# Kernel tuning notes

Hardware: AMD Instinct MI355X
Metric: run time of the kernel (lower is better)

## Reference

```python
import jax, jax.numpy as jnp
import numpy as np

N = 100000
E = 1600000
IN_CH = 64
HID = 32


def _gatv2(x, src, dst, wl, bl, wr, br, att, bias, heads, out_ch, concat):
    # GATv2Conv (PyG semantics, share_weights=False, negative_slope=0.2,
    # self-loops already appended to src/dst by caller).
    n = x.shape[0]
    xl = (x @ wl + bl).reshape(n, heads, out_ch)  # source transform
    xr = (x @ wr + br).reshape(n, heads, out_ch)  # target transform
    xj = xl[src]                                   # [E, H, C]
    xi = xr[dst]
    e = jax.nn.leaky_relu(xi + xj, negative_slope=0.2)
    alpha = jnp.einsum('ehc,hc->eh', e, att)       # [E, H]
    amax = jax.ops.segment_max(alpha, dst, num_segments=n)
    alpha = jnp.exp(alpha - amax[dst])
    denom = jax.ops.segment_sum(alpha, dst, num_segments=n)
    alpha = alpha / (denom[dst] + 1e-16)
    out = jax.ops.segment_sum(alpha[:, :, None] * xj, dst, num_segments=n)
    out = out.reshape(n, heads * out_ch) if concat else out.mean(axis=1)
    return out + bias


def setup_inputs() -> dict:
    key = jax.random.key(0)
    ks = jax.random.split(key, 20)
    s = 0.1
    d = {
        'x': jax.random.normal(ks[0], (N, IN_CH), jnp.float32),
        'edge_index': jax.random.randint(ks[1], (2, E), 0, N, jnp.int32),
        # conv1: in=64 -> heads=4, C=32, concat
        'w1l': s * jax.random.normal(ks[2], (IN_CH, 4 * HID), jnp.float32),
        'b1l': jnp.zeros((4 * HID,), jnp.float32),
        'w1r': s * jax.random.normal(ks[3], (IN_CH, 4 * HID), jnp.float32),
        'b1r': jnp.zeros((4 * HID,), jnp.float32),
        'a1': s * jax.random.normal(ks[4], (4, HID), jnp.float32),
        'c1': jnp.zeros((4 * HID,), jnp.float32),
        # conv2: in=128 -> heads=2, C=32, concat
        'w2l': s * jax.random.normal(ks[5], (4 * HID, 2 * HID), jnp.float32),
        'b2l': jnp.zeros((2 * HID,), jnp.float32),
        'w2r': s * jax.random.normal(ks[6], (4 * HID, 2 * HID), jnp.float32),
        'b2r': jnp.zeros((2 * HID,), jnp.float32),
        'a2': s * jax.random.normal(ks[7], (2, HID), jnp.float32),
        'c2': jnp.zeros((2 * HID,), jnp.float32),
        # conv3: in=64 -> heads=1, C=32, mean (concat=False)
        'w3l': s * jax.random.normal(ks[8], (2 * HID, HID), jnp.float32),
        'b3l': jnp.zeros((HID,), jnp.float32),
        'w3r': s * jax.random.normal(ks[9], (2 * HID, HID), jnp.float32),
        'b3r': jnp.zeros((HID,), jnp.float32),
        'a3': s * jax.random.normal(ks[10], (1, HID), jnp.float32),
        'c3': jnp.zeros((HID,), jnp.float32),
        # MLP head 32 -> 16 -> 2
        'wm1': s * jax.random.normal(ks[11], (HID, HID // 2), jnp.float32),
        'bm1': jnp.zeros((HID // 2,), jnp.float32),
        'wm2': s * jax.random.normal(ks[12], (HID // 2, 2), jnp.float32),
        'bm2': jnp.zeros((2,), jnp.float32),
    }
    return d


def reference(x, edge_index,
              w1l, b1l, w1r, b1r, a1, c1,
              w2l, b2l, w2r, b2r, a2, c2,
              w3l, b3l, w3r, b3r, a3, c3,
              wm1, bm1, wm2, bm2):
    n = x.shape[0]
    loop = jnp.arange(n, dtype=edge_index.dtype)
    src = jnp.concatenate([edge_index[0], loop])  # add_self_loops=True (PyG default)
    dst = jnp.concatenate([edge_index[1], loop])
    h = jax.nn.relu(_gatv2(x, src, dst, w1l, b1l, w1r, b1r, a1, c1, 4, HID, True))
    h = jax.nn.relu(_gatv2(h, src, dst, w2l, b2l, w2r, b2r, a2, c2, 2, HID, True))
    h = jax.nn.relu(_gatv2(h, src, dst, w3l, b3l, w3r, b3r, a3, c3, 1, HID, False))
    raw = jax.nn.relu(h @ wm1 + bm1) @ wm2 + bm2
    v_mag = jax.nn.sigmoid(raw[:, 0]) + 0.5
    v_angle = jnp.tanh(raw[:, 1]) * 180.0
    return jnp.stack([v_mag, v_angle], axis=1)
```

## Files before the change

### kernel.cpp

```cpp
#include <hip/hip_runtime.h>
#include <hip/hip_fp16.h>


constexpr int N = 100000;
constexpr int E = 1600000;
constexpr int S = 48;

constexpr int NBUK = (N + 127) >> 7;
constexpr int BCAP = 384;
constexpr int EPB = 8192;
constexpr int BIN_B = (E + EPB - 1) / EPB;
constexpr int XMM_B = (N + 127) / 128;

typedef _Float16 half8_t __attribute__((ext_vector_type(8)));
typedef _Float16 half4_t __attribute__((ext_vector_type(4)));
typedef _Float16 h2 __attribute__((ext_vector_type(2)));
typedef float f32x4 __attribute__((ext_vector_type(4)));


template <int NT>
__device__ __forceinline__ void bin_body(const int* __restrict__ ei,
                                         int* __restrict__ bcnt,
                                         unsigned* __restrict__ bbuf,
                                         int blk, int cls) {
  __shared__ int hist[NBUK];
  const int tid = threadIdx.x;
  const int e0 = blk * EPB;
  for (int i = tid; i < NBUK; i += NT) hist[i] = 0;
  __syncthreads();
  #pragma unroll 4
  for (int j = 0; j < EPB / NT; ++j) {
    const int e = e0 + j * NT + tid;
    if (e < E) atomicAdd(&hist[ei[E + e] >> 7], 1);
  }
  __syncthreads();
  for (int i = tid; i < NBUK; i += NT) {
    const int h = hist[i];
    hist[i] = h ? atomicAdd(&bcnt[i * 8 + cls], h) : 0;
  }
  __syncthreads();
  #pragma unroll 4
  for (int j = 0; j < EPB / NT; ++j) {
    const int e = e0 + j * NT + tid;
    if (e < E) {
      const int src = ei[e];
      const int dst = ei[E + e];
      const int b = dst >> 7;
      const int pos = atomicAdd(&hist[b], 1);
      if (pos < BCAP)
        bbuf[(size_t)(b * 8 + cls) * BCAP + pos] =
            ((unsigned)(dst & 127) << 17) | (unsigned)src;
    }
  }
}


__global__ __launch_bounds__(256) void k_insert(const int* __restrict__ bcnt,
                                                const unsigned* __restrict__ bbuf,
                                                int* __restrict__ deg,
                                                int* __restrict__ ebuf) {
  __shared__ int cnt[128];
  const int b = blockIdx.x;
  const int tid = threadIdx.x;
  const int node0 = b * 128 + tid;
  if (tid < 128) {
    cnt[tid] = 1;
    if (node0 < N) ebuf[node0 * S] = node0;
  }
  __syncthreads();
  #pragma unroll 1
  for (int c = 0; c < 8; ++c) {
    const int n = min(bcnt[b * 8 + c], BCAP);
    const unsigned* arr = bbuf + (size_t)(b * 8 + c) * BCAP;
    for (int i = tid; i < n; i += 256) {
      const unsigned ent = arr[i];
      const int dlo = (int)(ent >> 17);
      const int src = (int)(ent & 0x1FFFFu);
      const int pos = atomicAdd(&cnt[dlo], 1);
      if (pos < S) ebuf[(b * 128 + dlo) * S + pos] = src;
    }
  }
  __syncthreads();
  if (tid < 128 && node0 < N) deg[node0] = cnt[tid];
}


template <int K, int M>
__device__ __forceinline__ void wprep_body(const float* __restrict__ src,
                                           __half* __restrict__ dst, int blk) {
  const int idx = blk * 256 + threadIdx.x;
  const int k = idx / M;
  const int m = idx % M;
  ((_Float16*)dst)[m * K + (k ^ ((m & 7) << 3))] = (_Float16)src[idx];
}

__global__ __launch_bounds__(256) void k_wprep(
    const float* w1l, const float* w1r, const float* w2l, const float* w2r,
    const float* w3l, const float* w3r,
    __half* o1l, __half* o1r, __half* o2l, __half* o2r,
    __half* o3l, __half* o3r) {
  int b = blockIdx.x;
  if      (b < 32)  wprep_body<64, 128>(w1l, o1l, b);
  else if (b < 64)  wprep_body<64, 128>(w1r, o1r, b - 32);
  else if (b < 96)  wprep_body<128, 64>(w2l, o2l, b - 64);
  else if (b < 128) wprep_body<128, 64>(w2r, o2r, b - 96);
  else if (b < 136) wprep_body<64, 32>(w3l, o3l, b - 128);
  else              wprep_body<64, 32>(w3r, o3r, b - 136);
}


template <int K, int M, bool FP16IN>
__device__ __forceinline__ void xmm_body(const void* __restrict__ xin,
                                         const __half* __restrict__ wtl,
                                         const __half* __restrict__ wtr,
                                         const float* __restrict__ bl,
                                         const float* __restrict__ br,
                                         __half* __restrict__ Aout,
                                         __half* __restrict__ Bout, int blk) {
  constexpr int NPB = 128;
  constexpr int XSZ = NPB * K;
  constexpr int WSZ = M * K;
  constexpr int KS = K / 32;
  constexpr int CT = M / 16;
  constexpr int PSZ = (XSZ + 2 * WSZ) > (NPB * M) ? (XSZ + 2 * WSZ) : (NPB * M);
  __shared__ _Float16 pool[PSZ];

  const int tid = threadIdx.x;
  const int node0 = blk * NPB;

  if constexpr (!FP16IN) {
    const float* x = (const float*)xin;
    for (int i = tid; i < NPB * (K / 4); i += 512) {
      const int row = i / (K / 4);
      const int c4 = i % (K / 4);
      const int grow = min(node0 + row, N - 1);
      float4 v = reinterpret_cast<const float4*>(x)[(size_t)grow * (K / 4) + c4];
      const int k0 = c4 * 4;
      const int hidx = row * K + (k0 ^ ((row & 7) << 3));
      *reinterpret_cast<half4_t*>(&pool[hidx]) =
          (half4_t){(_Float16)v.x, (_Float16)v.y, (_Float16)v.z, (_Float16)v.w};
    }
  } else {
    const uint4* x = (const uint4*)xin;
    for (int i = tid; i < NPB * (K / 8); i += 512) {
      const int row = i / (K / 8);
      const int c8 = i % (K / 8);
      const int grow = min(node0 + row, N - 1);
      uint4 v = x[(size_t)grow * (K / 8) + c8];
      const int k0 = c8 * 8;
      *reinterpret_cast<uint4*>(&pool[row * K + (k0 ^ ((row & 7) << 3))]) = v;
    }
  }
  for (int i = tid; i < WSZ / 8; i += 512) {
    reinterpret_cast<uint4*>(&pool[XSZ])[i] =
        reinterpret_cast<const uint4*>(wtl)[i];
    reinterpret_cast<uint4*>(&pool[XSZ + WSZ])[i] =
        reinterpret_cast<const uint4*>(wtr)[i];
  }
  __syncthreads();

  const int lane = tid & 63;
  const int wid = tid >> 6;
  const int r0 = wid * 16;

  half8_t af[KS];
  #pragma unroll
  for (int ks = 0; ks < KS; ++ks) {
    const int row = r0 + (lane & 15);
    const int k0 = ks * 32 + (lane >> 4) * 8;
    af[ks] = *reinterpret_cast<const half8_t*>(
        &pool[row * K + (k0 ^ ((row & 7) << 3))]);
  }

  f32x4 accl[CT], accr[CT];
  #pragma unroll
  for (int ct = 0; ct < CT; ++ct) {
    accl[ct] = (f32x4){0.f, 0.f, 0.f, 0.f};
    accr[ct] = (f32x4){0.f, 0.f, 0.f, 0.f};
  }

  #pragma unroll
  for (int ct = 0; ct < CT; ++ct) {
    #pragma unroll
    for (int ks = 0; ks < KS; ++ks) {
      const int col = ct * 16 + (lane & 15);
      const int k0 = ks * 32 + (lane >> 4) * 8;
      const int hb = col * K + (k0 ^ ((col & 7) << 3));
      half8_t bfl = *reinterpret_cast<const half8_t*>(&pool[XSZ + hb]);
      accl[ct] = __builtin_amdgcn_mfma_f32_16x16x32_f16(af[ks], bfl, accl[ct], 0, 0, 0);
      half8_t bfr = *reinterpret_cast<const half8_t*>(&pool[XSZ + WSZ + hb]);
      accr[ct] = __builtin_amdgcn_mfma_f32_16x16x32_f16(af[ks], bfr, accr[ct], 0, 0, 0);
    }
  }

  __syncthreads();
  #pragma unroll
  for (int ct = 0; ct < CT; ++ct) {
    const int col = ct * 16 + (lane & 15);
    const float bb = bl[col];
    #pragma unroll
    for (int r = 0; r < 4; ++r) {
      const int row = r0 + (lane >> 4) * 4 + r;
      pool[row * M + col] = (_Float16)(accl[ct][r] + bb);
    }
  }
  __syncthreads();
  for (int i = tid; i < NPB * (M / 8); i += 512) {
    const int row = i / (M / 8);
    const int j = i % (M / 8);
    const int g = node0 + row;
    if (g < N)
      reinterpret_cast<uint4*>(Aout + (size_t)g * M)[j] =
          reinterpret_cast<uint4*>(&pool[row * M])[j];
  }
  __syncthreads();
  #pragma unroll
  for (int ct = 0; ct < CT; ++ct) {
    const int col = ct * 16 + (lane & 15);
    const float bb = br[col];
    #pragma unroll
    for (int r = 0; r < 4; ++r) {
      const int row = r0 + (lane >> 4) * 4 + r;
      pool[row * M + col] = (_Float16)(accr[ct][r] + bb);
    }
  }
  __syncthreads();
  for (int i = tid; i < NPB * (M / 8); i += 512) {
    const int row = i / (M / 8);
    const int j = i % (M / 8);
    const int g = node0 + row;
    if (g < N)
      reinterpret_cast<uint4*>(Bout + (size_t)g * M)[j] =
          reinterpret_cast<uint4*>(&pool[row * M])[j];
  }
}


__global__ __launch_bounds__(512) void k_front(const float* __restrict__ x,
                                               const __half* __restrict__ t1l,
                                               const __half* __restrict__ t1r,
                                               const float* __restrict__ b1l,
                                               const float* __restrict__ b1r,
                                               __half* __restrict__ A,
                                               __half* __restrict__ B,
                                               const int* __restrict__ ei,
                                               int* __restrict__ bcnt,
                                               unsigned* __restrict__ bbuf) {
  const int blk = blockIdx.x;
  if (blk < XMM_B) {
    xmm_body<64, 128, false>(x, t1l, t1r, b1l, b1r, A, B, blk);
    return;
  }
  bin_body<512>(ei, bcnt, bbuf, blk - XMM_B, blk & 7);
}


template <int K, int M, bool FP16IN>
__global__ __launch_bounds__(512) void k_xmm(const void* __restrict__ xin,
                                             const __half* __restrict__ wtl,
                                             const __half* __restrict__ wtr,
                                             const float* __restrict__ bl,
                                             const float* __restrict__ br,
                                             __half* __restrict__ Aout,
                                             __half* __restrict__ Bout) {
  xmm_body<K, M, FP16IN>(xin, wtl, wtr, bl, br, Aout, Bout, blockIdx.x);
}


template <int CTRL>
__device__ __forceinline__ float dpp_add(float x) {
  return x + __builtin_bit_cast(float,
      __builtin_amdgcn_update_dpp(0, __builtin_bit_cast(int, x),
                                  CTRL, 0xF, 0xF, true));
}

template <int H>
__global__ __launch_bounds__(256) void k_gat(const __half* __restrict__ xl,
                                             const __half* __restrict__ xr,
                                             const float* __restrict__ att,
                                             const float* __restrict__ bias,
                                             const int* __restrict__ deg,
                                             const int* __restrict__ ebuf,
                                             void* __restrict__ outv,
                                             const float* __restrict__ wm1,
                                             const float* __restrict__ bm1,
                                             const float* __restrict__ wm2,
                                             const float* __restrict__ bm2) {
  constexpr int F = H * 32;
  constexpr int F8 = F / 8;
  constexpr int LPE = F8;
  constexpr int EPI = 64 / LPE;
  constexpr float LOG2E = 1.44269504088896f;
  const int lane = threadIdx.x & 63;
  const int node = (blockIdx.x * blockDim.x + threadIdx.x) >> 6;
  if (node >= N) return;
  const int li = lane & (LPE - 1);
  const int eg = lane / LPE;

  const uint4* xl4 = reinterpret_cast<const uint4*>(xl);
  const uint4* xr4 = reinterpret_cast<const uint4*>(xr);

  const uint4 xiraw = xr4[(unsigned)node * F8 + li];
  h2 xi2[4];
  xi2[0] = __builtin_bit_cast(h2, xiraw.x);
  xi2[1] = __builtin_bit_cast(h2, xiraw.y);
  xi2[2] = __builtin_bit_cast(h2, xiraw.z);
  xi2[3] = __builtin_bit_cast(h2, xiraw.w);

  const float4 at0 = reinterpret_cast<const float4*>(att)[li * 2];
  const float4 at1 = reinterpret_cast<const float4*>(att)[li * 2 + 1];
  h2 at2[4];
  at2[0] = (h2){(_Float16)(at0.x * LOG2E), (_Float16)(at0.y * LOG2E)};
  at2[1] = (h2){(_Float16)(at0.z * LOG2E), (_Float16)(at0.w * LOG2E)};
  at2[2] = (h2){(_Float16)(at1.x * LOG2E), (_Float16)(at1.y * LOG2E)};
  at2[3] = (h2){(_Float16)(at1.z * LOG2E), (_Float16)(at1.w * LOG2E)};
  const h2 c02 = {(_Float16)0.2f, (_Float16)0.2f};

  float4 acc0 = make_float4(0.f, 0.f, 0.f, 0.f);
  float4 acc1 = make_float4(0.f, 0.f, 0.f, 0.f);
  float l = 0.f;

  const int* row = ebuf + node * S;
  const int dn = min(deg[node], S);
  const int last = dn - 1;
  const int iters = (dn + EPI - 1) / EPI;

  auto process = [&](const uint4& raw, bool valid) {
    h2 xj0 = __builtin_bit_cast(h2, raw.x);
    h2 xj1 = __builtin_bit_cast(h2, raw.y);
    h2 xj2 = __builtin_bit_cast(h2, raw.z);
    h2 xj3 = __builtin_bit_cast(h2, raw.w);
    float t = 0.f;
    h2 v;
    v = xi2[0] + xj0; v = __builtin_elementwise_max(v, v * c02);
    t = __builtin_amdgcn_fdot2(at2[0], v, t, false);
    v = xi2[1] + xj1; v = __builtin_elementwise_max(v, v * c02);
    t = __builtin_amdgcn_fdot2(at2[1], v, t, false);
    v = xi2[2] + xj2; v = __builtin_elementwise_max(v, v * c02);
    t = __builtin_amdgcn_fdot2(at2[2], v, t, false);
    v = xi2[3] + xj3; v = __builtin_elementwise_max(v, v * c02);
    t = __builtin_amdgcn_fdot2(at2[3], v, t, false);
    t = dpp_add<0xB1>(t);
    t = dpp_add<0x4E>(t);
    float pm = valid ? exp2f(t) : 0.f;
    l += pm;
    acc0.x = fmaf(pm, (float)xj0[0], acc0.x);
    acc0.y = fmaf(pm, (float)xj0[1], acc0.y);
    acc0.z = fmaf(pm, (float)xj1[0], acc0.z);
    acc0.w = fmaf(pm, (float)xj1[1], acc0.w);
    acc1.x = fmaf(pm, (float)xj2[0], acc1.x);
    acc1.y = fmaf(pm, (float)xj2[1], acc1.y);
    acc1.z = fmaf(pm, (float)xj3[0], acc1.z);
    acc1.w = fmaf(pm, (float)xj3[1], acc1.w);
  };

  int i = eg;
  bool vA = i < dn;
  int s0 = row[min(i, last)];
  i += EPI;
  uint4 xjA = xl4[(unsigned)s0 * F8 + li];
  bool vB = i < dn;
  int sN = row[min(i, last)];
  i += EPI;
  uint4 xjB;

  for (int it = 0; it < iters; it += 2) {
    xjB = xl4[(unsigned)sN * F8 + li];
    bool vn = i < dn;
    sN = row[min(i, last)];
    i += EPI;
    process(xjA, vA);
    vA = vn;
    xjA = xl4[(unsigned)sN * F8 + li];
    vn = i < dn;
    sN = row[min(i, last)];
    i += EPI;
    process(xjB, vB);
    vB = vn;
  }

  #pragma unroll
  for (int ofs = LPE; ofs < 64; ofs <<= 1) {
    acc0.x += __shfl_xor(acc0.x, ofs);
    acc0.y += __shfl_xor(acc0.y, ofs);
    acc0.z += __shfl_xor(acc0.z, ofs);
    acc0.w += __shfl_xor(acc0.w, ofs);
    acc1.x += __shfl_xor(acc1.x, ofs);
    acc1.y += __shfl_xor(acc1.y, ofs);
    acc1.z += __shfl_xor(acc1.z, ofs);
    acc1.w += __shfl_xor(acc1.w, ofs);
    l      += __shfl_xor(l, ofs);
  }

  if constexpr (H != 1) {
    __half* out = (__half*)outv;
    if (lane < LPE) {
      const float inv = 1.f / (l + 1e-16f);
      const float4 bv0 = reinterpret_cast<const float4*>(bias)[li * 2];
      const float4 bv1 = reinterpret_cast<const float4*>(bias)[li * 2 + 1];
      float r[8];
      r[0] = fmaxf(acc0.x * inv + bv0.x, 0.f);
      r[1] = fmaxf(acc0.y * inv + bv0.y, 0.f);
      r[2] = fmaxf(acc0.z * inv + bv0.z, 0.f);
      r[3] = fmaxf(acc0.w * inv + bv0.w, 0.f);
      r[4] = fmaxf(acc1.x * inv + bv1.x, 0.f);
      r[5] = fmaxf(acc1.y * inv + bv1.y, 0.f);
      r[6] = fmaxf(acc1.z * inv + bv1.z, 0.f);
      r[7] = fmaxf(acc1.w * inv + bv1.w, 0.f);
      uint4 o;
      #pragma unroll
      for (int p = 0; p < 4; ++p) {
        const h2 hh = {(_Float16)r[2 * p], (_Float16)r[2 * p + 1]};
        (&o.x)[p] = __builtin_bit_cast(unsigned, hh);
      }
      reinterpret_cast<uint4*>(out)[(unsigned)node * F8 + li] = o;
    }
  } else {
    __shared__ float hsh[4][32];
    if (lane < LPE) {
      const float inv = 1.f / (l + 1e-16f);
      const float4 bv0 = reinterpret_cast<const float4*>(bias)[li * 2];
      const float4 bv1 = reinterpret_cast<const float4*>(bias)[li * 2 + 1];
      float* hr = &hsh[threadIdx.x >> 6][li * 8];
      hr[0] = fmaxf(acc0.x * inv + bv0.x, 0.f);
      hr[1] = fmaxf(acc0.y * inv + bv0.y, 0.f);
      hr[2] = fmaxf(acc0.z * inv + bv0.z, 0.f);
      hr[3] = fmaxf(acc0.w * inv + bv0.w, 0.f);
      hr[4] = fmaxf(acc1.x * inv + bv1.x, 0.f);
      hr[5] = fmaxf(acc1.y * inv + bv1.y, 0.f);
      hr[6] = fmaxf(acc1.z * inv + bv1.z, 0.f);
      hr[7] = fmaxf(acc1.w * inv + bv1.w, 0.f);
    }
    __syncthreads();
    const int n = threadIdx.x >> 6;
    const int j = lane & 15;
    const int q = lane >> 4;
    float a = 0.f;
    #pragma unroll
    for (int k = 0; k < 8; ++k)
      a += hsh[n][q * 8 + k] * wm1[(q * 8 + k) * 16 + j];
    a += __shfl_xor(a, 16);
    a += __shfl_xor(a, 32);
    a = fmaxf(a + bm1[j], 0.f);
    float p0 = a * wm2[j * 2];
    float p1 = a * wm2[j * 2 + 1];
    #pragma unroll
    for (int ofs = 1; ofs < 16; ofs <<= 1) {
      p0 += __shfl_xor(p0, ofs);
      p1 += __shfl_xor(p1, ofs);
    }
    if (lane == 0) {
      float* out = (float*)outv;
      const float vm = 1.f / (1.f + __expf(-(p0 + bm2[0]))) + 0.5f;
      const float va = tanhf(p1 + bm2[1]) * 180.f;
      out[(size_t)node * 2]     = vm;
      out[(size_t)node * 2 + 1] = va;
    }
  }
}


extern "C" void kernel_launch(void* const* d_in, const int* in_sizes, int n_in,
                              void* d_out, int out_size, void* d_ws, size_t ws_size,
                              hipStream_t stream) {
  const float* x   = (const float*)d_in[0];
  const int*   ei  = (const int*)d_in[1];
  const float* w1l = (const float*)d_in[2];
  const float* b1l = (const float*)d_in[3];
  const float* w1r = (const float*)d_in[4];
  const float* b1r = (const float*)d_in[5];
  const float* a1  = (const float*)d_in[6];
  const float* c1  = (const float*)d_in[7];
  const float* w2l = (const float*)d_in[8];
  const float* b2l = (const float*)d_in[9];
  const float* w2r = (const float*)d_in[10];
  const float* b2r = (const float*)d_in[11];
  const float* a2  = (const float*)d_in[12];
  const float* c2  = (const float*)d_in[13];
  const float* w3l = (const float*)d_in[14];
  const float* b3l = (const float*)d_in[15];
  const float* w3r = (const float*)d_in[16];
  const float* b3r = (const float*)d_in[17];
  const float* a3  = (const float*)d_in[18];
  const float* c3  = (const float*)d_in[19];
  const float* wm1 = (const float*)d_in[20];
  const float* bm1 = (const float*)d_in[21];
  const float* wm2 = (const float*)d_in[22];
  const float* bm2 = (const float*)d_in[23];
  float* outp = (float*)d_out;
  (void)in_sizes; (void)n_in; (void)out_size; (void)ws_size;

  char* ws = (char*)d_ws;
  size_t o = 0;
  auto take = [&](size_t bytes) {
    char* p = ws + o;
    o = (o + bytes + 255) & ~(size_t)255;
    return p;
  };
  int* deg       = (int*)take((size_t)N * sizeof(int));
  int* ebuf      = (int*)take((size_t)N * S * sizeof(int));
  int* bcnt      = (int*)take((size_t)NBUK * 8 * sizeof(int));
  unsigned* bbuf = (unsigned*)take((size_t)NBUK * 8 * BCAP * sizeof(unsigned));
  __half* A      = (__half*)take((size_t)N * 128 * sizeof(__half));
  __half* B      = (__half*)take((size_t)N * 128 * sizeof(__half));
  __half* Cb     = (__half*)take((size_t)N * 128 * sizeof(__half));
  __half* t1l    = (__half*)take(128 * 64 * sizeof(__half));
  __half* t1r    = (__half*)take(128 * 64 * sizeof(__half));
  __half* t2l    = (__half*)take(64 * 128 * sizeof(__half));
  __half* t2r    = (__half*)take(64 * 128 * sizeof(__half));
  __half* t3l    = (__half*)take(32 * 64 * sizeof(__half));
  __half* t3r    = (__half*)take(32 * 64 * sizeof(__half));

  hipMemsetAsync(bcnt, 0, (size_t)NBUK * 8 * sizeof(int), stream);
  k_wprep<<<144, 256, 0, stream>>>(w1l, w1r, w2l, w2r, w3l, w3r,
                                   t1l, t1r, t2l, t2r, t3l, t3r);

  k_front<<<XMM_B + BIN_B, 512, 0, stream>>>(x, t1l, t1r, b1l, b1r, A, B,
                                             ei, bcnt, bbuf);
  k_insert<<<NBUK, 256, 0, stream>>>(bcnt, bbuf, deg, ebuf);

  k_gat<4><<<N / 4, 256, 0, stream>>>(A, B, a1, c1, deg, ebuf, Cb,
                                      nullptr, nullptr, nullptr, nullptr);

  k_xmm<128, 64, true><<<XMM_B, 512, 0, stream>>>(Cb, t2l, t2r, b2l, b2r, A, B);
  k_gat<2><<<N / 4, 256, 0, stream>>>(A, B, a2, c2, deg, ebuf, Cb,
                                      nullptr, nullptr, nullptr, nullptr);

  k_xmm<64, 32, true><<<XMM_B, 512, 0, stream>>>(Cb, t3l, t3r, b3l, b3r, A, B);
  k_gat<1><<<N / 4, 256, 0, stream>>>(A, B, a3, c3, deg, ebuf, outp,
                                      wm1, bm1, wm2, bm2);
}
```

Baseline: 367.2 us.

## Fuse layer-3 linear transforms into layer-2 GAT epilogue and drop memset

Layer 3's source and target projections (64->32 each) now run inside the layer-2 GAT kernel's epilogue, using fdot2 on the per-node hidden vector staged in shared memory. This removes one k_xmm launch and the round trip of the layer-2 output through global memory. The bcnt memset moves into k_wprep, and k_xmm loads the left and right weights into shared memory one after the other, halving weight LDS so occupancy can rise. The cost is extra per-node epilogue work and uncoalesced per-lane global weight reads in the GAT kernel.

```diff
diff --git a/kernel.cpp b/kernel.cpp
--- a/kernel.cpp
+++ b/kernel.cpp
@@ -98,7 +98,9 @@
     const float* w1l, const float* w1r, const float* w2l, const float* w2r,
     const float* w3l, const float* w3r,
     __half* o1l, __half* o1r, __half* o2l, __half* o2r,
-    __half* o3l, __half* o3r) {
+    __half* o3l, __half* o3r, int* bcnt) {
+  const int gi = blockIdx.x * 256 + threadIdx.x;
+  if (gi < NBUK * 8) bcnt[gi] = 0;
   int b = blockIdx.x;
   if      (b < 32)  wprep_body<64, 128>(w1l, o1l, b);
   else if (b < 64)  wprep_body<64, 128>(w1r, o1r, b - 32);
@@ -122,7 +124,7 @@
   constexpr int WSZ = M * K;
   constexpr int KS = K / 32;
   constexpr int CT = M / 16;
-  constexpr int PSZ = (XSZ + 2 * WSZ) > (NPB * M) ? (XSZ + 2 * WSZ) : (NPB * M);
+  constexpr int PSZ = (XSZ + WSZ) > (NPB * M) ? (XSZ + WSZ) : (NPB * M);
   __shared__ _Float16 pool[PSZ];
 
   const int tid = threadIdx.x;
@@ -151,12 +153,9 @@
       *reinterpret_cast<uint4*>(&pool[row * K + (k0 ^ ((row & 7) << 3))]) = v;
     }
   }
-  for (int i = tid; i < WSZ / 8; i += 512) {
+  for (int i = tid; i < WSZ / 8; i += 512)
     reinterpret_cast<uint4*>(&pool[XSZ])[i] =
         reinterpret_cast<const uint4*>(wtl)[i];
-    reinterpret_cast<uint4*>(&pool[XSZ + WSZ])[i] =
-        reinterpret_cast<const uint4*>(wtr)[i];
-  }
   __syncthreads();
 
   const int lane = tid & 63;
@@ -185,11 +184,25 @@
     for (int ks = 0; ks < KS; ++ks) {
       const int col = ct * 16 + (lane & 15);
       const int k0 = ks * 32 + (lane >> 4) * 8;
-      const int hb = col * K + (k0 ^ ((col & 7) << 3));
-      half8_t bfl = *reinterpret_cast<const half8_t*>(&pool[XSZ + hb]);
-      accl[ct] = __builtin_amdgcn_mfma_f32_16x16x32_f16(af[ks], bfl, accl[ct], 0, 0, 0);
-      half8_t bfr = *reinterpret_cast<const half8_t*>(&pool[XSZ + WSZ + hb]);
-      accr[ct] = __builtin_amdgcn_mfma_f32_16x16x32_f16(af[ks], bfr, accr[ct], 0, 0, 0);
+      half8_t bf = *reinterpret_cast<const half8_t*>(
+          &pool[XSZ + col * K + (k0 ^ ((col & 7) << 3))]);
+      accl[ct] = __builtin_amdgcn_mfma_f32_16x16x32_f16(af[ks], bf, accl[ct], 0, 0, 0);
+    }
+  }
+  __syncthreads();
+  for (int i = tid; i < WSZ / 8; i += 512)
+    reinterpret_cast<uint4*>(&pool[XSZ])[i] =
+        reinterpret_cast<const uint4*>(wtr)[i];
+  __syncthreads();
+  #pragma unroll
+  for (int ct = 0; ct < CT; ++ct) {
+    #pragma unroll
+    for (int ks = 0; ks < KS; ++ks) {
+      const int col = ct * 16 + (lane & 15);
+      const int k0 = ks * 32 + (lane >> 4) * 8;
+      half8_t bf = *reinterpret_cast<const half8_t*>(
+          &pool[XSZ + col * K + (k0 ^ ((col & 7) << 3))]);
+      accr[ct] = __builtin_amdgcn_mfma_f32_16x16x32_f16(af[ks], bf, accr[ct], 0, 0, 0);
     }
   }
 
@@ -274,18 +287,21 @@
                                   CTRL, 0xF, 0xF, true));
 }
 
-template <int H>
+template <int H, int MODE>
 __global__ __launch_bounds__(256) void k_gat(const __half* __restrict__ xl,
                                              const __half* __restrict__ xr,
                                              const float* __restrict__ att,
                                              const float* __restrict__ bias,
                                              const int* __restrict__ deg,
                                              const int* __restrict__ ebuf,
-                                             void* __restrict__ outv,
-                                             const float* __restrict__ wm1,
-                                             const float* __restrict__ bm1,
-                                             const float* __restrict__ wm2,
-                                             const float* __restrict__ bm2) {
+                                             void* __restrict__ out0,
+                                             void* __restrict__ out1,
+                                             const __half* __restrict__ hw0,
+                                             const __half* __restrict__ hw1,
+                                             const float* __restrict__ p0,
+                                             const float* __restrict__ p1,
+                                             const float* __restrict__ p2,
+                                             const float* __restrict__ p3) {
   constexpr int F = H * 32;
   constexpr int F8 = F / 8;
   constexpr int LPE = F8;
@@ -392,8 +408,8 @@
     l      += __shfl_xor(l, ofs);
   }
 
-  if constexpr (H != 1) {
-    __half* out = (__half*)outv;
+  if constexpr (MODE == 0) {
+    __half* out = (__half*)out0;
     if (lane < LPE) {
       const float inv = 1.f / (l + 1e-16f);
       const float4 bv0 = reinterpret_cast<const float4*>(bias)[li * 2];
@@ -415,6 +431,56 @@
       }
       reinterpret_cast<uint4*>(out)[(unsigned)node * F8 + li] = o;
     }
+  } else if constexpr (MODE == 1) {
+    __shared__ _Float16 hsh[4][64];
+    const int n = threadIdx.x >> 6;
+    if (lane < LPE) {
+      const float inv = 1.f / (l + 1e-16f);
+      const float4 bv0 = reinterpret_cast<const float4*>(bias)[li * 2];
+      const float4 bv1 = reinterpret_cast<const float4*>(bias)[li * 2 + 1];
+      float r[8];
+      r[0] = fmaxf(acc0.x * inv + bv0.x, 0.f);
+      r[1] = fmaxf(acc0.y * inv + bv0.y, 0.f);
+      r[2] = fmaxf(acc0.z * inv + bv0.z, 0.f);
+      r[3] = fmaxf(acc0.w * inv + bv0.w, 0.f);
+      r[4] = fmaxf(acc1.x * inv + bv1.x, 0.f);
+      r[5] = fmaxf(acc1.y * inv + bv1.y, 0.f);
+      r[6] = fmaxf(acc1.z * inv + bv1.z, 0.f);
+      r[7] = fmaxf(acc1.w * inv + bv1.w, 0.f);
+      uint4 o;
+      #pragma unroll
+      for (int p = 0; p < 4; ++p) {
+        const h2 hh = {(_Float16)r[2 * p], (_Float16)r[2 * p + 1]};
+        (&o.x)[p] = __builtin_bit_cast(unsigned, hh);
+      }
+      *reinterpret_cast<uint4*>(&hsh[n][li * 8]) = o;
+    }
+    __syncthreads();
+    {
+      const int m = lane & 31;
+      const bool rs = lane >= 32;
+      const __half* wt = rs ? hw1 : hw0;
+      const float* bb = rs ? p1 : p0;
+      const uint4* w4 = reinterpret_cast<const uint4*>(wt) + m * 8;
+      const int sw = m & 7;
+      float acc = 0.f;
+      #pragma unroll
+      for (int jj = 0; jj < 8; ++jj) {
+        const uint4 w = w4[jj];
+        const uint4 hv = *reinterpret_cast<const uint4*>(&hsh[n][(jj ^ sw) << 3]);
+        acc = __builtin_amdgcn_fdot2(__builtin_bit_cast(h2, w.x),
+                                     __builtin_bit_cast(h2, hv.x), acc, false);
+        acc = __builtin_amdgcn_fdot2(__builtin_bit_cast(h2, w.y),
+                                     __builtin_bit_cast(h2, hv.y), acc, false);
+        acc = __builtin_amdgcn_fdot2(__builtin_bit_cast(h2, w.z),
+                                     __builtin_bit_cast(h2, hv.z), acc, false);
+        acc = __builtin_amdgcn_fdot2(__builtin_bit_cast(h2, w.w),
+                                     __builtin_bit_cast(h2, hv.w), acc, false);
+      }
+      acc += bb[m];
+      __half* dst = rs ? (__half*)out1 : (__half*)out0;
+      dst[(unsigned)node * 32 + m] = (__half)(_Float16)acc;
+    }
   } else {
     __shared__ float hsh[4][32];
     if (lane < LPE) {
@@ -438,21 +504,21 @@
     float a = 0.f;
     #pragma unroll
     for (int k = 0; k < 8; ++k)
-      a += hsh[n][q * 8 + k] * wm1[(q * 8 + k) * 16 + j];
+      a += hsh[n][q * 8 + k] * p0[(q * 8 + k) * 16 + j];
     a += __shfl_xor(a, 16);
     a += __shfl_xor(a, 32);
-    a = fmaxf(a + bm1[j], 0.f);
-    float p0 = a * wm2[j * 2];
-    float p1 = a * wm2[j * 2 + 1];
+    a = fmaxf(a + p1[j], 0.f);
+    float q0 = a * p2[j * 2];
+    float q1 = a * p2[j * 2 + 1];
     #pragma unroll
     for (int ofs = 1; ofs < 16; ofs <<= 1) {
-      p0 += __shfl_xor(p0, ofs);
-      p1 += __shfl_xor(p1, ofs);
+      q0 += __shfl_xor(q0, ofs);
+      q1 += __shfl_xor(q1, ofs);
     }
     if (lane == 0) {
-      float* out = (float*)outv;
-      const float vm = 1.f / (1.f + __expf(-(p0 + bm2[0]))) + 0.5f;
-      const float va = tanhf(p1 + bm2[1]) * 180.f;
+      float* out = (float*)out0;
+      const float vm = 1.f / (1.f + __expf(-(q0 + p3[0]))) + 0.5f;
+      const float va = tanhf(q1 + p3[1]) * 180.f;
       out[(size_t)node * 2]     = vm;
       out[(size_t)node * 2 + 1] = va;
     }
@@ -510,23 +576,27 @@
   __half* t2r    = (__half*)take(64 * 128 * sizeof(__half));
   __half* t3l    = (__half*)take(32 * 64 * sizeof(__half));
   __half* t3r    = (__half*)take(32 * 64 * sizeof(__half));
-
-  hipMemsetAsync(bcnt, 0, (size_t)NBUK * 8 * sizeof(int), stream);
+  __half* A3     = Cb;
+  __half* B3     = Cb + (size_t)N * 32;
+
   k_wprep<<<144, 256, 0, stream>>>(w1l, w1r, w2l, w2r, w3l, w3r,
-                                   t1l, t1r, t2l, t2r, t3l, t3r);
+                                   t1l, t1r, t2l, t2r, t3l, t3r, bcnt);
 
   k_front<<<XMM_B + BIN_B, 512, 0, stream>>>(x, t1l, t1r, b1l, b1r, A, B,
                                              ei, bcnt, bbuf);
   k_insert<<<NBUK, 256, 0, stream>>>(bcnt, bbuf, deg, ebuf);
 
-  k_gat<4><<<N / 4, 256, 0, stream>>>(A, B, a1, c1, deg, ebuf, Cb,
-                                      nullptr, nullptr, nullptr, nullptr);
+  k_gat<4, 0><<<N / 4, 256, 0, stream>>>(A, B, a1, c1, deg, ebuf, Cb, nullptr,
+                                         nullptr, nullptr,
+                                         nullptr, nullptr, nullptr, nullptr);
 
   k_xmm<128, 64, true><<<XMM_B, 512, 0, stream>>>(Cb, t2l, t2r, b2l, b2r, A, B);
-  k_gat<2><<<N / 4, 256, 0, stream>>>(A, B, a2, c2, deg, ebuf, Cb,
-                                      nullptr, nullptr, nullptr, nullptr);
-
-  k_xmm<64, 32, true><<<XMM_B, 512, 0, stream>>>(Cb, t3l, t3r, b3l, b3r, A, B);
-  k_gat<1><<<N / 4, 256, 0, stream>>>(A, B, a3, c3, deg, ebuf, outp,
-                                      wm1, bm1, wm2, bm2);
-}
+
+  k_gat<2, 1><<<N / 4, 256, 0, stream>>>(A, B, a2, c2, deg, ebuf, A3, B3,
+                                         t3l, t3r,
+                                         b3l, b3r, nullptr, nullptr);
+
+  k_gat<1, 2><<<N / 4, 256, 0, stream>>>(A3, B3, a3, c3, deg, ebuf, outp,
+                                         nullptr, nullptr, nullptr,
+                                         wm1, bm1, wm2, bm2);
+}
```

Result: slower. 432.7 us (+17.8%).
